# Kernel optimization log

Measured on AMD Instinct MI355X. Metric: run time of the kernel, lower is better.

## Reference

```python
import jax, jax.numpy as jnp
import numpy as np

E, B, T = 8, 8, 1024
DIN = 640    # hidden_state_dim + conf_dim
DH = 1024    # 2 * hidden_state_dim
DOUT = 128   # 1024 // num_experts (slicing=True)
CODE = 256
TAU = 0.1
IMPORTANCE_REG = 0.01
EPS = 1e-8


def setup_inputs() -> dict:
    key = jax.random.key(0)
    ks = jax.random.split(key, 9)
    h = jax.random.normal(ks[0], (B, T, DIN), jnp.float32)
    code_emb = jax.random.normal(ks[1], (B, T, CODE), jnp.float32)
    u = jax.random.uniform(ks[2], (B, T, E), jnp.float32, 1e-6, 1.0 - 1e-6)
    gumbel_noise = -jnp.log(-jnp.log(u))
    code_anchor = jax.random.normal(ks[3], (E, CODE), jnp.float32)
    feature_importance = jax.random.normal(ks[4], (E, DIN), jnp.float32)
    W1 = jax.random.normal(ks[5], (E, DIN, DH), jnp.float32) * 0.02
    b1 = jax.random.normal(ks[6], (E, DH), jnp.float32) * 0.02
    W2 = jax.random.normal(ks[7], (E, DH, DOUT), jnp.float32) * 0.02
    b2 = jax.random.normal(ks[8], (E, DOUT), jnp.float32) * 0.02
    return {"h": h, "code_emb": code_emb, "gumbel_noise": gumbel_noise,
            "code_anchor": code_anchor, "feature_importance": feature_importance,
            "W1": W1, "b1": b1, "W2": W2, "b2": b2}


def _l2norm(x, axis):
    n = jnp.sqrt(jnp.sum(x * x, axis=axis, keepdims=True))
    return x / jnp.maximum(n, 1e-12)


def reference(h, code_emb, gumbel_noise, code_anchor, feature_importance, W1, b1, W2, b2):
    # router logits: cosine similarity between code_emb and code anchors  [B,T,E]
    anchor_n = _l2norm(code_anchor, axis=1)
    code_n = _l2norm(code_emb, axis=-1)
    router_logits = jnp.einsum('btd,ed->bte', code_n, anchor_n)
    # gumbel-softmax, tau=0.1, hard=False (noise provided for determinism)
    expert_weights = jax.nn.softmax((router_logits + gumbel_noise) / TAU, axis=-1)  # [B,T,E]
    # temperature-scaled importance softmax; importance_temperature=0.5, clamp no-op
    temp = jnp.clip(jnp.float32(0.5), 0.1, 5.0)
    importance = jax.nn.softmax(feature_importance / temp, axis=1)  # [E,DIN]
    # per-expert importance-weighted inputs [B,E,T,DIN]
    weighted_h = h[:, None, :, :] * importance[None, :, None, :]
    # all experts as one batched 2-layer MLP (exact GELU like torch nn.GELU)
    hid = jax.nn.gelu(jnp.einsum('betd,edh->beth', weighted_h, W1) + b1[None, :, None, :],
                      approximate=False)
    expert_outputs = jnp.einsum('beth,eho->beto', hid, W2) + b2[None, :, None, :]  # [B,E,T,DOUT]
    # slicing combine: expert i fills output slice [i*DOUT:(i+1)*DOUT], scaled by its gate
    gated = expert_outputs.transpose(0, 2, 1, 3) * expert_weights[..., None]  # [B,T,E,DOUT]
    full_output = gated.reshape(B, T, E * DOUT)  # [B,T,1024]
    # routing aux loss
    expert_counts = expert_weights.sum(0)  # [T,E]
    expert_load = expert_counts / (expert_counts.sum() + EPS)
    routing_loss = 0.5 * (jnp.std(expert_counts, ddof=1)
                          + (-expert_load * jnp.log(expert_load + EPS)).sum())
    imp_entropy = -(importance * jnp.log(importance + EPS)).sum(-1)  # [E]
    aux_loss = routing_loss + IMPORTANCE_REG * imp_entropy.mean()
    # diversity loss on raw feature_importance
    sim = feature_importance @ feature_importance.T  # [E,E]
    off = sim * (1.0 - jnp.eye(E, dtype=sim.dtype))
    diversity_loss = (off ** 2).sum() / (E * (E - 1))
    imp_mean = importance.mean(-1)
    imp_std = jnp.std(importance, axis=-1, ddof=1)
    return full_output, aux_loss, diversity_loss, imp_entropy, imp_mean, imp_std
```

## Files before the change

kernel.cpp:

```cpp
#include <hip/hip_runtime.h>
#include <math.h>

#define DIN 640
#define DH 1024
#define DOUT 128
#define CODEDIM 256
#define NE 8
#define NB 8
#define NT 1024
#define NTOK 8192
#define TAU_INV 10.0f
#define FEPS 1e-8f

#define AUX_OFF  8388608
#define DIV_OFF  8388609
#define ENT_OFF  8388610
#define MEAN_OFF 8388618
#define STD_OFF  8388626

typedef __bf16 bf16;
typedef bf16 bf16x8 __attribute__((ext_vector_type(8)));
typedef float f32x4 __attribute__((ext_vector_type(4)));

__device__ __forceinline__ float gelu(float x) {
  return 0.5f * x * (1.0f + erff(x * 0.70710678118654752f));
}

#define BAR() do { asm volatile("" ::: "memory"); __builtin_amdgcn_s_barrier(); asm volatile("" ::: "memory"); } while(0)
#define VMCNT6 asm volatile("s_waitcnt vmcnt(6)" ::: "memory")
#define VMCNT0 asm volatile("s_waitcnt vmcnt(0)" ::: "memory")

__device__ __forceinline__ void gload16(const void* g, void* l) {
  __builtin_amdgcn_global_load_lds(
      (const __attribute__((address_space(1))) unsigned int*)g,
      (__attribute__((address_space(3))) unsigned int*)l, 16, 0, 0);
}

__device__ __forceinline__ float blk_sum(float v, float* sb) {
  #pragma unroll
  for (int o = 32; o > 0; o >>= 1) v += __shfl_down(v, o, 64);
  __syncthreads();
  if ((threadIdx.x & 63) == 0) sb[threadIdx.x >> 6] = v;
  __syncthreads();
  float tot = 0.f;
  int nw = blockDim.x >> 6;
  for (int i = 0; i < nw; ++i) tot += sb[i];
  return tot;
}

__device__ __forceinline__ float blk_max(float v, float* sb) {
  #pragma unroll
  for (int o = 32; o > 0; o >>= 1) v = fmaxf(v, __shfl_down(v, o, 64));
  __syncthreads();
  if ((threadIdx.x & 63) == 0) sb[threadIdx.x >> 6] = v;
  __syncthreads();
  float m = -3.0e38f;
  int nw = blockDim.x >> 6;
  for (int i = 0; i < nw; ++i) m = fmaxf(m, sb[i]);
  return m;
}

__global__ void k_imp(const float* __restrict__ fi, float* __restrict__ imp,
                      float* __restrict__ out) {
  __shared__ float sb[8];
  int e = blockIdx.x, tid = threadIdx.x;
  int d2v = tid + 512;
  float v0 = fi[e*DIN + tid] * 2.0f;
  float v1 = fi[e*DIN + tid + 256] * 2.0f;
  float v2 = (d2v < DIN) ? fi[e*DIN + d2v] * 2.0f : -3.0e38f;
  float m = blk_max(fmaxf(v0, fmaxf(v1, v2)), sb);
  float e0 = expf(v0 - m), e1 = expf(v1 - m);
  float e2 = (d2v < DIN) ? expf(v2 - m) : 0.f;
  float s = blk_sum(e0 + e1 + e2, sb);
  float inv = 1.0f / s;
  float p0 = e0*inv, p1 = e1*inv, p2 = e2*inv;
  imp[e*DIN + tid] = p0;
  imp[e*DIN + tid + 256] = p1;
  if (d2v < DIN) imp[e*DIN + d2v] = p2;
  float ok2 = (d2v < DIN) ? 1.f : 0.f;
  float sp  = p0 + p1 + ok2*p2;
  float sp2 = p0*p0 + p1*p1 + ok2*p2*p2;
  float se  = p0*logf(p0 + FEPS) + p1*logf(p1 + FEPS) + ok2*p2*logf(p2 + FEPS);
  sp  = blk_sum(sp, sb);
  sp2 = blk_sum(sp2, sb);
  se  = blk_sum(se, sb);
  if (tid == 0) {
    out[ENT_OFF + e]  = -se;
    out[MEAN_OFF + e] = sp * (1.0f/DIN);
    float var = (sp2 - sp*sp*(1.0f/DIN)) * (1.0f/(DIN-1));
    out[STD_OFF + e]  = sqrtf(fmaxf(var, 0.f));
  }
}

__global__ void k_anchor_div(const float* __restrict__ ca, const float* __restrict__ fi,
                             float* __restrict__ anch, float* __restrict__ out) {
  __shared__ float sb[8];
  __shared__ float sd[256];
  int tid = threadIdx.x;
  for (int e = 0; e < NE; ++e) {
    float x = ca[e*CODEDIM + tid];
    float ss = blk_sum(x*x, sb);
    anch[e*CODEDIM + tid] = x / fmaxf(sqrtf(ss), 1e-12f);
  }
  int p = tid >> 2, q = tid & 3;
  int i = p >> 3, j = p & 7;
  float dot = 0.f;
  for (int d = q*160; d < q*160 + 160; ++d) dot += fi[i*DIN + d] * fi[j*DIN + d];
  sd[tid] = dot;
  __syncthreads();
  if (tid < 64) {
    float s = sd[tid*4] + sd[tid*4+1] + sd[tid*4+2] + sd[tid*4+3];
    int ii = tid >> 3, jj = tid & 7;
    float val = (ii != jj) ? s*s : 0.f;
    #pragma unroll
    for (int o = 32; o > 0; o >>= 1) val += __shfl_down(val, o, 64);
    if (tid == 0) out[DIV_OFF] = val * (1.0f/56.0f);
  }
}

__global__ void k_transpose(const float* __restrict__ src, bf16* __restrict__ dst,
                            int R, int C, const float* __restrict__ scale) {
  __shared__ float tile[64][65];
  int c0 = blockIdx.x*64, r0 = blockIdx.y*64;
  int ee = blockIdx.z;
  const float* s = src + (size_t)ee*R*C;
  bf16* d = dst + (size_t)ee*C*R;
  int tx = threadIdx.x & 63, ty = threadIdx.x >> 6;
  #pragma unroll
  for (int p = 0; p < 16; ++p) {
    int r = p*4 + ty;
    tile[r][tx] = s[(size_t)(r0 + r)*C + c0 + tx];
  }
  __syncthreads();
  float sc = scale ? scale[(size_t)ee*R + r0 + tx] : 1.0f;
  #pragma unroll
  for (int p = 0; p < 16; ++p) {
    int cr = p*4 + ty;
    d[(size_t)(c0 + cr)*R + r0 + tx] = (bf16)(tile[tx][cr] * sc);
  }
}

__global__ void k_h2b(const float* __restrict__ h, bf16* __restrict__ xb) {
  size_t i = (size_t)blockIdx.x*256 + threadIdx.x;
  const float4* p = (const float4*)(h + i*8);
  float4 v0 = p[0], v1 = p[1];
  bf16x8 o;
  o[0]=(bf16)v0.x; o[1]=(bf16)v0.y; o[2]=(bf16)v0.z; o[3]=(bf16)v0.w;
  o[4]=(bf16)v1.x; o[5]=(bf16)v1.y; o[6]=(bf16)v1.z; o[7]=(bf16)v1.w;
  *(bf16x8*)(xb + i*8) = o;
}

__global__ void k_router(const float* __restrict__ ce, const float* __restrict__ gn,
                         const float* __restrict__ anch, float* __restrict__ ew) {
  __shared__ float anc[NE*CODEDIM];
  int tid = threadIdx.x;
  for (int i2 = tid; i2 < NE*CODEDIM; i2 += 256) anc[i2] = anch[i2];
  __syncthreads();
  int wv = tid >> 6, lane = tid & 63;
  int token = blockIdx.x*4 + wv;
  float4 x = *(const float4*)(ce + (size_t)token*CODEDIM + lane*4);
  float ss = x.x*x.x + x.y*x.y + x.z*x.z + x.w*x.w;
  #pragma unroll
  for (int o = 1; o < 64; o <<= 1) ss += __shfl_xor(ss, o, 64);
  float inv = 1.0f / fmaxf(sqrtf(ss), 1e-12f);
  const float* g = gn + (size_t)token*NE;
  float z[8];
  float m = -3.0e38f;
  #pragma unroll
  for (int e2 = 0; e2 < NE; ++e2) {
    const float* a = anc + e2*CODEDIM + lane*4;
    float d = x.x*a[0] + x.y*a[1] + x.z*a[2] + x.w*a[3];
    #pragma unroll
    for (int o = 1; o < 64; o <<= 1) d += __shfl_xor(d, o, 64);
    z[e2] = (d*inv + g[e2]) * TAU_INV;
    m = fmaxf(m, z[e2]);
  }
  float ssum = 0.f;
  float pz[8];
  #pragma unroll
  for (int e2 = 0; e2 < NE; ++e2) { pz[e2] = expf(z[e2] - m); ssum += pz[e2]; }
  float num = 0.f;
  #pragma unroll
  for (int e2 = 0; e2 < NE; ++e2) num = (lane == e2) ? pz[e2] : num;
  if (lane < NE) ew[(size_t)token*NE + lane] = num / ssum;
}

#define G1_LDS 34816
__global__ __launch_bounds__(256, 3)
void k_g1(const bf16* __restrict__ xb, const bf16* __restrict__ w1t,
          const float* __restrict__ b1, bf16* __restrict__ Hb, int ebase) {
  __shared__ __align__(16) char L[G1_LDS];
  const int bid = blockIdx.x;
  const int el = bid & 3, e = ebase + el;
  const int nt = (bid >> 2) & 7, mt = bid >> 5;
  const int M0 = mt * 128, N0 = nt * 128;
  const int tid = threadIdx.x;
  const int lane = tid & 63, w = tid >> 6;
  const int l15 = lane & 15, g4 = lane >> 4;
  const int wr = w >> 1, wc = w & 1;

  const char* gAsrc[4];
  const char* gBsrc[4];
  #pragma unroll
  for (int j = 0; j < 4; ++j) {
    unsigned p = (unsigned)((w*4 + j)*1024 + lane*16);
    unsigned q = p ^ (((p >> 7) & 7u) << 4);
    gAsrc[j] = (const char*)xb + (size_t)(M0 + (int)(q >> 7))*(DIN*2) + (q & 127u);
    gBsrc[j] = (const char*)w1t + (size_t)(e*DH + N0 + (int)(q >> 7))*(DIN*2) + (q & 127u);
  }

  unsigned afOff[4][2], bfOff[4][2];
  #pragma unroll
  for (int mi = 0; mi < 4; ++mi)
    #pragma unroll
    for (int kk = 0; kk < 2; ++kk) {
      int row = wr*64 + mi*16 + l15;
      int slot = kk*4 + g4;
      afOff[mi][kk] = (unsigned)(row*128 + ((slot ^ (row & 7)) << 4));
    }
  #pragma unroll
  for (int ni = 0; ni < 4; ++ni)
    #pragma unroll
    for (int kk = 0; kk < 2; ++kk) {
      int row = wc*64 + ni*16 + l15;
      int slot = kk*4 + g4;
      bfOff[ni][kk] = (unsigned)(16384 + row*128 + ((slot ^ (row & 7)) << 4));
    }

  f32x4 acc[4][4] = {};
  for (int t = 0; t < 10; ++t) {
    if (t) BAR();
    size_t ko = (size_t)t * 128;
    #pragma unroll
    for (int j = 0; j < 4; ++j) {
      gload16(gAsrc[j] + ko, L + (w*4 + j)*1024);
      gload16(gBsrc[j] + ko, L + 16384 + (w*4 + j)*1024);
    }
    VMCNT0;
    BAR();
    #pragma unroll
    for (int kk = 0; kk < 2; ++kk) {
      bf16x8 af[4], bfr[4];
      #pragma unroll
      for (int mi = 0; mi < 4; ++mi) af[mi] = *(const bf16x8*)(L + afOff[mi][kk]);
      #pragma unroll
      for (int ni = 0; ni < 4; ++ni) bfr[ni] = *(const bf16x8*)(L + bfOff[ni][kk]);
      #pragma unroll
      for (int mi = 0; mi < 4; ++mi)
        #pragma unroll
        for (int ni = 0; ni < 4; ++ni)
          acc[mi][ni] = __builtin_amdgcn_mfma_f32_16x16x32_bf16(
              af[mi], bfr[ni], acc[mi][ni], 0, 0, 0);
    }
  }
  BAR();
  float b1v[4];
  #pragma unroll
  for (int ni = 0; ni < 4; ++ni)
    b1v[ni] = b1[e*DH + N0 + wc*64 + ni*16 + l15];
  #pragma unroll
  for (int mi = 0; mi < 4; ++mi)
    #pragma unroll
    for (int ni = 0; ni < 4; ++ni)
      #pragma unroll
      for (int r = 0; r < 4; ++r) {
        float v = gelu(acc[mi][ni][r] + b1v[ni]);
        int row = wr*64 + mi*16 + g4*4 + r;
        int col = wc*64 + ni*16 + l15;
        *(bf16*)(L + row*272 + col*2) = (bf16)v;
      }
  __syncthreads();
  #pragma unroll
  for (int j = 0; j < 8; ++j) {
    int c = j*256 + tid;
    int row = c >> 4, slot = c & 15;
    bf16x8 v = *(const bf16x8*)(L + row*272 + slot*16);
    *(bf16x8*)((char*)Hb + (size_t)(el*NTOK + M0 + row)*(DH*2) + (size_t)N0*2 + slot*16) = v;
  }
}

__global__ __launch_bounds__(256, 3)
void k_g2(const bf16* __restrict__ Hb, const bf16* __restrict__ w2t,
          const float* __restrict__ b2, const float* __restrict__ ew,
          float* __restrict__ out, int ebase) {
  __shared__ __align__(16) char L[49152];
  const int bid = blockIdx.x;
  const int el = bid & 3, e = ebase + el;
  const int mt = bid >> 2;
  const int M0 = mt * 64;
  const int tid = threadIdx.x;
  const int lane = tid & 63, w = tid >> 6;
  const int l15 = lane & 15, g4 = lane >> 4;
  const int nb = w * 32;

  const char* gAsrc[2];
  #pragma unroll
  for (int j = 0; j < 2; ++j) {
    unsigned p = (unsigned)((w*2 + j)*1024 + lane*16);
    unsigned q = p ^ (((p >> 7) & 7u) << 4);
    gAsrc[j] = (const char*)Hb + (size_t)(el*NTOK + M0 + (int)(q >> 7))*(DH*2) + (q & 127u);
  }
  const char* gBsrc[4];
  #pragma unroll
  for (int j = 0; j < 4; ++j) {
    unsigned p = (unsigned)((w*4 + j)*1024 + lane*16);
    unsigned q = p ^ (((p >> 7) & 7u) << 4);
    gBsrc[j] = (const char*)w2t + (size_t)(e*DOUT + (int)(q >> 7))*(DH*2) + (q & 127u);
  }
  auto STAGE = [&](int buf, int t) {
    size_t ko = (size_t)t * 128;
    #pragma unroll
    for (int j = 0; j < 2; ++j)
      gload16(gAsrc[j] + ko, L + buf*8192 + (w*2 + j)*1024);
    #pragma unroll
    for (int j = 0; j < 4; ++j)
      gload16(gBsrc[j] + ko, L + 16384 + buf*16384 + (w*4 + j)*1024);
  };

  unsigned afOff[4][2], bfOff[2][2];
  #pragma unroll
  for (int mi = 0; mi < 4; ++mi)
    #pragma unroll
    for (int kk = 0; kk < 2; ++kk) {
      int row = mi*16 + l15;
      int slot = kk*4 + g4;
      afOff[mi][kk] = (unsigned)(row*128 + ((slot ^ (row & 7)) << 4));
    }
  #pragma unroll
  for (int ni = 0; ni < 2; ++ni)
    #pragma unroll
    for (int kk = 0; kk < 2; ++kk) {
      int row = nb + ni*16 + l15;
      int slot = kk*4 + g4;
      bfOff[ni][kk] = (unsigned)(row*128 + ((slot ^ (row & 7)) << 4));
    }

  f32x4 acc[4][2] = {};
  STAGE(0, 0);
  for (int t = 0; t < 16; ++t) {
    int buf = t & 1;
    if (t < 15) { STAGE(buf ^ 1, t + 1); VMCNT6; } else { VMCNT0; }
    BAR();
    const char* Ab = L + buf*8192;
    const char* Bb = L + 16384 + buf*16384;
    #pragma unroll
    for (int kk = 0; kk < 2; ++kk) {
      bf16x8 af[4], bfr[2];
      #pragma unroll
      for (int mi = 0; mi < 4; ++mi) af[mi] = *(const bf16x8*)(Ab + afOff[mi][kk]);
      #pragma unroll
      for (int ni = 0; ni < 2; ++ni) bfr[ni] = *(const bf16x8*)(Bb + bfOff[ni][kk]);
      #pragma unroll
      for (int mi = 0; mi < 4; ++mi)
        #pragma unroll
        for (int ni = 0; ni < 2; ++ni)
          acc[mi][ni] = __builtin_amdgcn_mfma_f32_16x16x32_bf16(
              af[mi], bfr[ni], acc[mi][ni], 0, 0, 0);
    }
    BAR();
  }
  float b2v[2];
  #pragma unroll
  for (int ni = 0; ni < 2; ++ni)
    b2v[ni] = b2[e*DOUT + nb + ni*16 + l15];
  float gt[4][4];
  #pragma unroll
  for (int mi = 0; mi < 4; ++mi)
    #pragma unroll
    for (int r = 0; r < 4; ++r)
      gt[mi][r] = ew[(size_t)(M0 + mi*16 + g4*4 + r)*NE + e];
  #pragma unroll
  for (int mi = 0; mi < 4; ++mi)
    #pragma unroll
    for (int ni = 0; ni < 2; ++ni)
      #pragma unroll
      for (int r = 0; r < 4; ++r) {
        int tok = M0 + mi*16 + g4*4 + r;
        int o = nb + ni*16 + l15;
        out[(size_t)tok*(NE*DOUT) + e*DOUT + o] = (acc[mi][ni][r] + b2v[ni]) * gt[mi][r];
      }
}

__global__ void k_counts(const float* __restrict__ ew, float* __restrict__ counts,
                         float* __restrict__ partials) {
  __shared__ float sb[4];
  int g2 = blockIdx.x*256 + threadIdx.x;
  float c = 0.f;
  #pragma unroll
  for (int b = 0; b < NB; ++b) c += ew[b*(NT*NE) + g2];
  counts[g2] = c;
  float tot = blk_sum(c, sb);
  if (threadIdx.x == 0) partials[blockIdx.x] = tot;
}

__global__ void k_aux(const float* __restrict__ counts, const float* __restrict__ partials,
                      float* __restrict__ out) {
  __shared__ float sb[4];
  int tid = threadIdx.x;
  float pv = (tid < 32) ? partials[tid] : 0.f;
  float total = blk_sum(pv, sb);
  float invt = 1.0f / (total + FEPS);
  float sq = 0.f, ent = 0.f;
  for (int i2 = tid; i2 < NT*NE; i2 += 256) {
    float c = counts[i2];
    sq += c*c;
    float ld = c * invt;
    ent -= ld * logf(ld + FEPS);
  }
  sq = blk_sum(sq, sb);
  ent = blk_sum(ent, sb);
  if (tid == 0) {
    float var = (sq - total*total*(1.0f/(NT*NE))) * (1.0f/(NT*NE - 1));
    float stdv = sqrtf(fmaxf(var, 0.f));
    float ment = 0.f;
    #pragma unroll
    for (int e2 = 0; e2 < NE; ++e2) ment += out[ENT_OFF + e2];
    ment *= (1.0f/NE);
    out[AUX_OFF] = 0.5f*(stdv + ent) + 0.01f*ment;
  }
}

extern "C" void kernel_launch(void* const* d_in, const int* in_sizes, int n_in,
                              void* d_out, int out_size, void* d_ws, size_t ws_size,
                              hipStream_t stream) {
  const float* h  = (const float*)d_in[0];
  const float* ce = (const float*)d_in[1];
  const float* gn = (const float*)d_in[2];
  const float* ca = (const float*)d_in[3];
  const float* fi = (const float*)d_in[4];
  const float* W1 = (const float*)d_in[5];
  const float* b1 = (const float*)d_in[6];
  const float* W2 = (const float*)d_in[7];
  const float* b2 = (const float*)d_in[8];
  float* out = (float*)d_out;
  char* ws = (char*)d_ws;
  bf16*  w1t      = (bf16*)(ws);
  bf16*  w2t      = (bf16*)(ws + 10485760);
  bf16*  xbuf     = (bf16*)(ws + 12582912);
  float* imp      = (float*)(ws + 23068672);
  float* anch     = (float*)(ws + 23089152);
  float* ew       = (float*)(ws + 23097344);
  float* counts   = (float*)(ws + 23359488);
  float* partials = (float*)(ws + 23392256);
  bf16*  Hbuf     = (bf16*)(ws + 23396352);

  k_imp<<<dim3(8), dim3(256), 0, stream>>>(fi, imp, out);
  k_anchor_div<<<dim3(1), dim3(256), 0, stream>>>(ca, fi, anch, out);
  k_transpose<<<dim3(16, 10, 8), dim3(256), 0, stream>>>(W1, w1t, 640, 1024, imp);
  k_transpose<<<dim3(2, 16, 8), dim3(256), 0, stream>>>(W2, w2t, 1024, 128, nullptr);
  k_h2b<<<dim3(2560), dim3(256), 0, stream>>>(h, xbuf);
  k_router<<<dim3(2048), dim3(256), 0, stream>>>(ce, gn, anch, ew);
  k_g1<<<dim3(2048), dim3(256), 0, stream>>>(xbuf, w1t, b1, Hbuf, 0);
  k_g2<<<dim3(512), dim3(256), 0, stream>>>(Hbuf, w2t, b2, ew, out, 0);
  k_g1<<<dim3(2048), dim3(256), 0, stream>>>(xbuf, w1t, b1, Hbuf, 4);
  k_g2<<<dim3(512), dim3(256), 0, stream>>>(Hbuf, w2t, b2, ew, out, 4);
  k_counts<<<dim3(32), dim3(256), 0, stream>>>(ew, counts, partials);
  k_aux<<<dim3(1), dim3(256), 0, stream>>>(counts, partials, out);
}
```

Baseline: 202.2 us.

## Fuse six preprocessing kernels into one block-dispatched prep kernel

Replaces the importance softmax, anchor normalisation/diversity, two weight transposes, h-to-bf16 cast and router kernels with a single launch that dispatches work by block index. The W1 transpose blocks recompute the importance softmax locally instead of reading a precomputed buffer, and router blocks normalise the anchors themselves, removing inter-kernel dependencies. This cuts five launches and their serialisation gaps, at the cost of redundant softmax and anchor-norm work in every block and a union of shared-memory footprints that may lower occupancy.

```diff
diff --git a/kernel.cpp b/kernel.cpp
--- a/kernel.cpp
+++ b/kernel.cpp
@@ -60,129 +60,165 @@
   return m;
 }
 
-__global__ void k_imp(const float* __restrict__ fi, float* __restrict__ imp,
-                      float* __restrict__ out) {
-  __shared__ float sb[8];
-  int e = blockIdx.x, tid = threadIdx.x;
-  int d2v = tid + 512;
-  float v0 = fi[e*DIN + tid] * 2.0f;
-  float v1 = fi[e*DIN + tid + 256] * 2.0f;
-  float v2 = (d2v < DIN) ? fi[e*DIN + d2v] * 2.0f : -3.0e38f;
-  float m = blk_max(fmaxf(v0, fmaxf(v1, v2)), sb);
-  float e0 = expf(v0 - m), e1 = expf(v1 - m);
-  float e2 = (d2v < DIN) ? expf(v2 - m) : 0.f;
-  float s = blk_sum(e0 + e1 + e2, sb);
-  float inv = 1.0f / s;
-  float p0 = e0*inv, p1 = e1*inv, p2 = e2*inv;
-  imp[e*DIN + tid] = p0;
-  imp[e*DIN + tid + 256] = p1;
-  if (d2v < DIN) imp[e*DIN + d2v] = p2;
-  float ok2 = (d2v < DIN) ? 1.f : 0.f;
-  float sp  = p0 + p1 + ok2*p2;
-  float sp2 = p0*p0 + p1*p1 + ok2*p2*p2;
-  float se  = p0*logf(p0 + FEPS) + p1*logf(p1 + FEPS) + ok2*p2*logf(p2 + FEPS);
-  sp  = blk_sum(sp, sb);
-  sp2 = blk_sum(sp2, sb);
-  se  = blk_sum(se, sb);
-  if (tid == 0) {
-    out[ENT_OFF + e]  = -se;
-    out[MEAN_OFF + e] = sp * (1.0f/DIN);
-    float var = (sp2 - sp*sp*(1.0f/DIN)) * (1.0f/(DIN-1));
-    out[STD_OFF + e]  = sqrtf(fmaxf(var, 0.f));
-  }
-}
-
-__global__ void k_anchor_div(const float* __restrict__ ca, const float* __restrict__ fi,
-                             float* __restrict__ anch, float* __restrict__ out) {
-  __shared__ float sb[8];
-  __shared__ float sd[256];
-  int tid = threadIdx.x;
-  for (int e = 0; e < NE; ++e) {
-    float x = ca[e*CODEDIM + tid];
-    float ss = blk_sum(x*x, sb);
-    anch[e*CODEDIM + tid] = x / fmaxf(sqrtf(ss), 1e-12f);
-  }
-  int p = tid >> 2, q = tid & 3;
-  int i = p >> 3, j = p & 7;
-  float dot = 0.f;
-  for (int d = q*160; d < q*160 + 160; ++d) dot += fi[i*DIN + d] * fi[j*DIN + d];
-  sd[tid] = dot;
-  __syncthreads();
-  if (tid < 64) {
-    float s = sd[tid*4] + sd[tid*4+1] + sd[tid*4+2] + sd[tid*4+3];
-    int ii = tid >> 3, jj = tid & 7;
-    float val = (ii != jj) ? s*s : 0.f;
-    #pragma unroll
-    for (int o = 32; o > 0; o >>= 1) val += __shfl_down(val, o, 64);
-    if (tid == 0) out[DIV_OFF] = val * (1.0f/56.0f);
-  }
-}
-
-__global__ void k_transpose(const float* __restrict__ src, bf16* __restrict__ dst,
-                            int R, int C, const float* __restrict__ scale) {
-  __shared__ float tile[64][65];
-  int c0 = blockIdx.x*64, r0 = blockIdx.y*64;
-  int ee = blockIdx.z;
-  const float* s = src + (size_t)ee*R*C;
-  bf16* d = dst + (size_t)ee*C*R;
-  int tx = threadIdx.x & 63, ty = threadIdx.x >> 6;
-  #pragma unroll
-  for (int p = 0; p < 16; ++p) {
-    int r = p*4 + ty;
-    tile[r][tx] = s[(size_t)(r0 + r)*C + c0 + tx];
-  }
-  __syncthreads();
-  float sc = scale ? scale[(size_t)ee*R + r0 + tx] : 1.0f;
-  #pragma unroll
-  for (int p = 0; p < 16; ++p) {
-    int cr = p*4 + ty;
-    d[(size_t)(c0 + cr)*R + r0 + tx] = (bf16)(tile[tx][cr] * sc);
-  }
-}
-
-__global__ void k_h2b(const float* __restrict__ h, bf16* __restrict__ xb) {
-  size_t i = (size_t)blockIdx.x*256 + threadIdx.x;
-  const float4* p = (const float4*)(h + i*8);
-  float4 v0 = p[0], v1 = p[1];
-  bf16x8 o;
-  o[0]=(bf16)v0.x; o[1]=(bf16)v0.y; o[2]=(bf16)v0.z; o[3]=(bf16)v0.w;
-  o[4]=(bf16)v1.x; o[5]=(bf16)v1.y; o[6]=(bf16)v1.z; o[7]=(bf16)v1.w;
-  *(bf16x8*)(xb + i*8) = o;
-}
-
-__global__ void k_router(const float* __restrict__ ce, const float* __restrict__ gn,
-                         const float* __restrict__ anch, float* __restrict__ ew) {
-  __shared__ float anc[NE*CODEDIM];
-  int tid = threadIdx.x;
-  for (int i2 = tid; i2 < NE*CODEDIM; i2 += 256) anc[i2] = anch[i2];
-  __syncthreads();
-  int wv = tid >> 6, lane = tid & 63;
-  int token = blockIdx.x*4 + wv;
-  float4 x = *(const float4*)(ce + (size_t)token*CODEDIM + lane*4);
-  float ss = x.x*x.x + x.y*x.y + x.z*x.z + x.w*x.w;
-  #pragma unroll
-  for (int o = 1; o < 64; o <<= 1) ss += __shfl_xor(ss, o, 64);
-  float inv = 1.0f / fmaxf(sqrtf(ss), 1e-12f);
-  const float* g = gn + (size_t)token*NE;
-  float z[8];
-  float m = -3.0e38f;
-  #pragma unroll
-  for (int e2 = 0; e2 < NE; ++e2) {
-    const float* a = anc + e2*CODEDIM + lane*4;
-    float d = x.x*a[0] + x.y*a[1] + x.z*a[2] + x.w*a[3];
-    #pragma unroll
-    for (int o = 1; o < 64; o <<= 1) d += __shfl_xor(d, o, 64);
-    z[e2] = (d*inv + g[e2]) * TAU_INV;
-    m = fmaxf(m, z[e2]);
-  }
-  float ssum = 0.f;
-  float pz[8];
-  #pragma unroll
-  for (int e2 = 0; e2 < NE; ++e2) { pz[e2] = expf(z[e2] - m); ssum += pz[e2]; }
-  float num = 0.f;
-  #pragma unroll
-  for (int e2 = 0; e2 < NE; ++e2) num = (lane == e2) ? pz[e2] : num;
-  if (lane < NE) ew[(size_t)token*NE + lane] = num / ssum;
+__global__ __launch_bounds__(256)
+void k_prep(const float* __restrict__ h, const float* __restrict__ ce,
+            const float* __restrict__ gn, const float* __restrict__ ca,
+            const float* __restrict__ fi, const float* __restrict__ W1,
+            const float* __restrict__ W2,
+            bf16* __restrict__ w1t, bf16* __restrict__ w2t,
+            bf16* __restrict__ xb, float* __restrict__ ew,
+            float* __restrict__ out) {
+  const int bid = blockIdx.x;
+  const int tid = threadIdx.x;
+  if (bid < 1280) {
+    __shared__ float tile[64][65];
+    __shared__ float sb[8];
+    __shared__ float red[2];
+    int c0 = (bid & 15) * 64;
+    int r0 = ((bid >> 4) % 10) * 64;
+    int ee = bid / 160;
+    const float* s = W1 + (size_t)ee*DIN*DH;
+    bf16* d = w1t + (size_t)ee*DH*DIN;
+    int i2v = tid + 512;
+    float v0 = fi[ee*DIN + tid] * 2.0f;
+    float v1 = fi[ee*DIN + tid + 256] * 2.0f;
+    float v2 = (i2v < DIN) ? fi[ee*DIN + i2v] * 2.0f : -3.0e38f;
+    float m = blk_max(fmaxf(v0, fmaxf(v1, v2)), sb);
+    float se = expf(v0 - m) + expf(v1 - m) + ((i2v < DIN) ? expf(v2 - m) : 0.f);
+    float ssum = blk_sum(se, sb);
+    if (tid == 0) { red[0] = m; red[1] = 1.0f / ssum; }
+    int tx = tid & 63, ty = tid >> 6;
+    #pragma unroll
+    for (int p = 0; p < 16; ++p) {
+      int r = p*4 + ty;
+      tile[r][tx] = s[(size_t)(r0 + r)*DH + c0 + tx];
+    }
+    __syncthreads();
+    float sc = expf(fi[ee*DIN + r0 + tx]*2.0f - red[0]) * red[1];
+    #pragma unroll
+    for (int p = 0; p < 16; ++p) {
+      int cr = p*4 + ty;
+      d[(size_t)(c0 + cr)*DIN + r0 + tx] = (bf16)(tile[tx][cr] * sc);
+    }
+  } else if (bid < 1536) {
+    __shared__ float tile[64][65];
+    int c = bid - 1280;
+    int c0 = (c & 1) * 64;
+    int r0 = ((c >> 1) & 15) * 64;
+    int ee = c >> 5;
+    const float* s = W2 + (size_t)ee*DH*DOUT;
+    bf16* d = w2t + (size_t)ee*DOUT*DH;
+    int tx = tid & 63, ty = tid >> 6;
+    #pragma unroll
+    for (int p = 0; p < 16; ++p) {
+      int r = p*4 + ty;
+      tile[r][tx] = s[(size_t)(r0 + r)*DOUT + c0 + tx];
+    }
+    __syncthreads();
+    #pragma unroll
+    for (int p = 0; p < 16; ++p) {
+      int cr = p*4 + ty;
+      d[(size_t)(c0 + cr)*DH + r0 + tx] = (bf16)tile[tx][cr];
+    }
+  } else if (bid < 4096) {
+    size_t i = (size_t)(bid - 1536)*256 + tid;
+    const float4* p = (const float4*)(h + i*8);
+    float4 u0 = p[0], u1 = p[1];
+    bf16x8 o;
+    o[0]=(bf16)u0.x; o[1]=(bf16)u0.y; o[2]=(bf16)u0.z; o[3]=(bf16)u0.w;
+    o[4]=(bf16)u1.x; o[5]=(bf16)u1.y; o[6]=(bf16)u1.z; o[7]=(bf16)u1.w;
+    *(bf16x8*)(xb + i*8) = o;
+  } else if (bid < 6144) {
+    __shared__ float anc[NE*CODEDIM];
+    __shared__ float sd[256];
+    __shared__ float invn[8];
+    int c = bid - 4096;
+    for (int i = tid; i < NE*CODEDIM; i += 256) anc[i] = ca[i];
+    __syncthreads();
+    {
+      int e8 = tid >> 5, base = e8*CODEDIM + (tid & 31)*8;
+      float ps = 0.f;
+      #pragma unroll
+      for (int j = 0; j < 8; ++j) { float v = anc[base + j]; ps += v*v; }
+      sd[tid] = ps;
+    }
+    __syncthreads();
+    if (tid < 8) {
+      float s2 = 0.f;
+      for (int j = 0; j < 32; ++j) s2 += sd[tid*32 + j];
+      invn[tid] = 1.0f / fmaxf(sqrtf(s2), 1e-12f);
+    }
+    __syncthreads();
+    int wv = tid >> 6, lane = tid & 63;
+    int token = c*4 + wv;
+    float4 x = *(const float4*)(ce + (size_t)token*CODEDIM + lane*4);
+    float ss = x.x*x.x + x.y*x.y + x.z*x.z + x.w*x.w;
+    #pragma unroll
+    for (int o = 1; o < 64; o <<= 1) ss += __shfl_xor(ss, o, 64);
+    float invx = 1.0f / fmaxf(sqrtf(ss), 1e-12f);
+    const float* g = gn + (size_t)token*NE;
+    float z[8];
+    float m = -3.0e38f;
+    #pragma unroll
+    for (int e2 = 0; e2 < NE; ++e2) {
+      const float* a = anc + e2*CODEDIM + lane*4;
+      float d = x.x*a[0] + x.y*a[1] + x.z*a[2] + x.w*a[3];
+      #pragma unroll
+      for (int o = 1; o < 64; o <<= 1) d += __shfl_xor(d, o, 64);
+      z[e2] = (d * invx * invn[e2] + g[e2]) * TAU_INV;
+      m = fmaxf(m, z[e2]);
+    }
+    float ssum = 0.f;
+    float pz[8];
+    #pragma unroll
+    for (int e2 = 0; e2 < NE; ++e2) { pz[e2] = expf(z[e2] - m); ssum += pz[e2]; }
+    float num = 0.f;
+    #pragma unroll
+    for (int e2 = 0; e2 < NE; ++e2) num = (lane == e2) ? pz[e2] : num;
+    if (lane < NE) ew[(size_t)token*NE + lane] = num / ssum;
+  } else if (bid < 6152) {
+    __shared__ float sb[8];
+    int e = bid - 6144;
+    int d2v = tid + 512;
+    float v0 = fi[e*DIN + tid] * 2.0f;
+    float v1 = fi[e*DIN + tid + 256] * 2.0f;
+    float v2 = (d2v < DIN) ? fi[e*DIN + d2v] * 2.0f : -3.0e38f;
+    float m = blk_max(fmaxf(v0, fmaxf(v1, v2)), sb);
+    float e0 = expf(v0 - m), e1 = expf(v1 - m);
+    float e2 = (d2v < DIN) ? expf(v2 - m) : 0.f;
+    float s = blk_sum(e0 + e1 + e2, sb);
+    float inv = 1.0f / s;
+    float p0 = e0*inv, p1 = e1*inv, p2 = e2*inv;
+    float ok2 = (d2v < DIN) ? 1.f : 0.f;
+    float sp  = p0 + p1 + ok2*p2;
+    float sp2 = p0*p0 + p1*p1 + ok2*p2*p2;
+    float sent = p0*logf(p0 + FEPS) + p1*logf(p1 + FEPS) + ok2*p2*logf(p2 + FEPS);
+    sp   = blk_sum(sp, sb);
+    sp2  = blk_sum(sp2, sb);
+    sent = blk_sum(sent, sb);
+    if (tid == 0) {
+      out[ENT_OFF + e]  = -sent;
+      out[MEAN_OFF + e] = sp * (1.0f/DIN);
+      float var = (sp2 - sp*sp*(1.0f/DIN)) * (1.0f/(DIN-1));
+      out[STD_OFF + e]  = sqrtf(fmaxf(var, 0.f));
+    }
+  } else {
+    __shared__ float sd[256];
+    int p = tid >> 2, q = tid & 3;
+    int i = p >> 3, j = p & 7;
+    float dot = 0.f;
+    for (int d = q*160; d < q*160 + 160; ++d) dot += fi[i*DIN + d] * fi[j*DIN + d];
+    sd[tid] = dot;
+    __syncthreads();
+    if (tid < 64) {
+      float s = sd[tid*4] + sd[tid*4+1] + sd[tid*4+2] + sd[tid*4+3];
+      int ii = tid >> 3, jj = tid & 7;
+      float val = (ii != jj) ? s*s : 0.f;
+      #pragma unroll
+      for (int o = 32; o > 0; o >>= 1) val += __shfl_down(val, o, 64);
+      if (tid == 0) out[DIV_OFF] = val * (1.0f/56.0f);
+    }
+  }
 }
 
 #define G1_LDS 34816
@@ -437,19 +473,13 @@
   bf16*  w1t      = (bf16*)(ws);
   bf16*  w2t      = (bf16*)(ws + 10485760);
   bf16*  xbuf     = (bf16*)(ws + 12582912);
-  float* imp      = (float*)(ws + 23068672);
-  float* anch     = (float*)(ws + 23089152);
   float* ew       = (float*)(ws + 23097344);
   float* counts   = (float*)(ws + 23359488);
   float* partials = (float*)(ws + 23392256);
   bf16*  Hbuf     = (bf16*)(ws + 23396352);
 
-  k_imp<<<dim3(8), dim3(256), 0, stream>>>(fi, imp, out);
-  k_anchor_div<<<dim3(1), dim3(256), 0, stream>>>(ca, fi, anch, out);
-  k_transpose<<<dim3(16, 10, 8), dim3(256), 0, stream>>>(W1, w1t, 640, 1024, imp);
-  k_transpose<<<dim3(2, 16, 8), dim3(256), 0, stream>>>(W2, w2t, 1024, 128, nullptr);
-  k_h2b<<<dim3(2560), dim3(256), 0, stream>>>(h, xbuf);
-  k_router<<<dim3(2048), dim3(256), 0, stream>>>(ce, gn, anch, ew);
+  k_prep<<<dim3(6153), dim3(256), 0, stream>>>(h, ce, gn, ca, fi, W1, W2,
+                                               w1t, w2t, xbuf, ew, out);
   k_g1<<<dim3(2048), dim3(256), 0, stream>>>(xbuf, w1t, b1, Hbuf, 0);
   k_g2<<<dim3(512), dim3(256), 0, stream>>>(Hbuf, w2t, b2, ew, out, 0);
   k_g1<<<dim3(2048), dim3(256), 0, stream>>>(xbuf, w1t, b1, Hbuf, 4);
```

New measurement: 187.6 us (median of 2 runs). 1.08x faster.
